# Optimization experiments

Measured on AMD Instinct MI355X. Metric: run time of the kernel, lower is better.

Reference implementation:

```python
import jax, jax.numpy as jnp
import numpy as np

H = 768
NH = 12
HD = H // NH  # 64
WINDOW = 64  # module's self.window_size; band keeps |i-j| <= WINDOW//2


def setup_inputs() -> dict:
    key = jax.random.key(0)
    ks = jax.random.split(key, 9)
    s = 0.02
    return {
        "hidden_states": jax.random.normal(ks[0], (4, 2048, H), dtype=jnp.float32),
        "Wq": jax.random.normal(ks[1], (H, H), dtype=jnp.float32) * s,
        "bq": jnp.zeros((H,), dtype=jnp.float32),
        "Wk": jax.random.normal(ks[2], (H, H), dtype=jnp.float32) * s,
        "bk": jnp.zeros((H,), dtype=jnp.float32),
        "Wv": jax.random.normal(ks[3], (H, H), dtype=jnp.float32) * s,
        "bv": jnp.zeros((H,), dtype=jnp.float32),
        "Wo": jax.random.normal(ks[4], (H, H), dtype=jnp.float32) * s,
        "bo": jnp.zeros((H,), dtype=jnp.float32),
    }


def _attn(hidden_states, Wq, bq, Wk, bk, Wv, bv, Wo, bo):
    B, S, _ = hidden_states.shape
    # projections (torch Linear uses y = x @ W.T + b; here W is stored already transposed)
    q = (hidden_states @ Wq + bq).reshape(B, S, NH, HD).transpose(0, 2, 1, 3)
    k = (hidden_states @ Wk + bk).reshape(B, S, NH, HD).transpose(0, 2, 1, 3)
    v = (hidden_states @ Wv + bv).reshape(B, S, NH, HD).transpose(0, 2, 1, 3)
    # dense scores [B, NH, S, S], faithful to the original O(S^2) computation
    scores = jnp.einsum("bhqd,bhkd->bhqk", q, k) / jnp.sqrt(jnp.float32(HD))
    # sliding-window band mask: keep j in [i - W//2, i + W//2]
    i = jnp.arange(S)[:, None]
    j = jnp.arange(S)[None, :]
    band = jnp.abs(i - j) <= (WINDOW // 2)
    scores = jnp.where(band[None, None, :, :], scores, jnp.float32(-1e9))
    probs = jax.nn.softmax(scores, axis=-1)
    ctx = jnp.einsum("bhqk,bhkd->bhqd", probs, v)
    ctx = ctx.transpose(0, 2, 1, 3).reshape(B, S, H)
    return ctx @ Wo + bo


def reference(hidden_states, Wq, bq, Wk, bk, Wv, bv, Wo, bo):
    return _attn(hidden_states, Wq, bq, Wk, bk, Wv, bv, Wo, bo)
```

## Files before the change

### kernel.cpp

```cpp
#include <hip/hip_runtime.h>
#include <hip/hip_bf16.h>

#define NHEAD 12
#define HD 64
#define SEQ 2048
#define NB 4
#define HDIM 768
#define MTOT (NB * SEQ)

typedef float f32x4 __attribute__((ext_vector_type(4)));
typedef float f32x16 __attribute__((ext_vector_type(16)));
typedef short s16x8 __attribute__((ext_vector_type(8)));
typedef unsigned short u16x8 __attribute__((ext_vector_type(8)));

__device__ inline unsigned short f2bf(float f) {
    union { float f; unsigned u; } v; v.f = f;
    unsigned r = v.u + 0x7fffu + ((v.u >> 16) & 1u);
    return (unsigned short)(r >> 16);
}
__device__ inline float bf2f(unsigned short u) {
    union { unsigned u; float f; } v; v.u = ((unsigned)u) << 16;
    return v.f;
}
__device__ inline unsigned pack_bf2(float a, float b) {
    return (unsigned)f2bf(a) | ((unsigned)f2bf(b) << 16);
}
__device__ inline s16x8 mk_frag(uint2 lo, uint2 hi) {
    union { unsigned u[4]; s16x8 v; } r;
    r.u[0] = lo.x; r.u[1] = lo.y; r.u[2] = hi.x; r.u[3] = hi.y;
    return r.v;
}
__device__ inline void gload_lds16(const unsigned short* g, void* lds_base) {
    __builtin_amdgcn_global_load_lds(
        (const __attribute__((address_space(1))) void*)g,
        (__attribute__((address_space(3))) void*)lds_base, 16, 0, 0);
}

#define MFMA(acc, a, b) \
    acc = __builtin_amdgcn_mfma_f32_16x16x32_bf16((a), (b), (acc), 0, 0, 0)
#define MFMA32(acc, a, b) \
    acc = __builtin_amdgcn_mfma_f32_32x32x16_bf16((a), (b), (acc), 0, 0, 0)

__global__ __launch_bounds__(256) void x_convert(
    const float* __restrict__ X, unsigned short* __restrict__ Xb)
{
    const int i = (blockIdx.x * 256 + threadIdx.x) * 8;
    float4 a = *(const float4*)(X + i);
    float4 b = *(const float4*)(X + i + 4);
    ushort4 wa, wb;
    wa.x = f2bf(a.x); wa.y = f2bf(a.y); wa.z = f2bf(a.z); wa.w = f2bf(a.w);
    wb.x = f2bf(b.x); wb.y = f2bf(b.y); wb.z = f2bf(b.z); wb.w = f2bf(b.w);
    *(ushort4*)(Xb + i) = wa;
    *(ushort4*)(Xb + i + 4) = wb;
}

__global__ __launch_bounds__(256) void w_transpose(
    const float* __restrict__ Wq, const float* __restrict__ Wk,
    const float* __restrict__ Wv, const float* __restrict__ Wo,
    unsigned short* __restrict__ Wt, unsigned short* __restrict__ Wot)
{
    __shared__ __align__(16) unsigned short ts[64][68];
    const int z = blockIdx.z;
    const float* W = (z == 0) ? Wq : (z == 1) ? Wk : (z == 2) ? Wv : Wo;
    unsigned short* D = (z < 3) ? (Wt + (size_t)z * HDIM * HDIM) : Wot;
    const int k0 = blockIdx.x * 64, n0 = blockIdx.y * 64;
    const int t = threadIdx.x;
    const int kr = (t >> 4) * 4;
    const int nc = (t & 15) * 4;
    #pragma unroll
    for (int r = 0; r < 4; r++) {
        float4 v = *(const float4*)(W + (size_t)(k0 + kr + r) * HDIM + n0 + nc);
        ushort4 w;
        w.x = f2bf(v.x); w.y = f2bf(v.y); w.z = f2bf(v.z); w.w = f2bf(v.w);
        *(ushort4*)&ts[kr + r][nc] = w;
    }
    __syncthreads();
    const int nr = t >> 2;
    const int kc = (t & 3) * 16;
    #pragma unroll
    for (int j4 = 0; j4 < 4; j4++) {
        ushort4 w;
        w.x = ts[kc + j4 * 4 + 0][nr];
        w.y = ts[kc + j4 * 4 + 1][nr];
        w.z = ts[kc + j4 * 4 + 2][nr];
        w.w = ts[kc + j4 * 4 + 3][nr];
        *(ushort4*)(D + (size_t)(n0 + nr) * HDIM + k0 + kc + j4 * 4) = w;
    }
}

template<int MODE>
__global__ __launch_bounds__(256) void gemm_kernel(
    const unsigned short* __restrict__ A,
    const unsigned short* __restrict__ Bt,
    const float* __restrict__ bias0, const float* __restrict__ bias1,
    const float* __restrict__ bias2,
    unsigned short* __restrict__ Qb, unsigned short* __restrict__ Kb,
    unsigned short* __restrict__ Vb, float* __restrict__ out)
{
    __shared__ __align__(16) unsigned short As[128 * 64];
    __shared__ __align__(16) unsigned short Bs[128 * 64];

    const int t = threadIdx.x;
    const int lane = t & 63;
    const int wid = t >> 6;
    const int wm = wid >> 1, wn = wid & 1;
    const int l31 = lane & 31;
    const int lh = lane >> 5;

    const int m0 = blockIdx.x * 128;
    const int n0 = blockIdx.y * 128;

    int srow[4], scol[4];
    #pragma unroll
    for (int i = 0; i < 4; i++) {
        const int p = i * 4096 + t * 16;
        const int row = p >> 7;
        const int cb = p & 127;
        srow[i] = row;
        scol[i] = (cb ^ ((row & 7) << 4)) >> 1;
    }

    f32x16 acc[2][2] = {};

    for (int k0 = 0; k0 < HDIM; k0 += 64) {
        __syncthreads();
        #pragma unroll
        for (int i = 0; i < 4; i++)
            gload_lds16(A + (size_t)(m0 + srow[i]) * HDIM + k0 + scol[i],
                        (char*)As + i * 4096 + wid * 1024);
        #pragma unroll
        for (int i = 0; i < 4; i++)
            gload_lds16(Bt + (size_t)(n0 + srow[i]) * HDIM + k0 + scol[i],
                        (char*)Bs + i * 4096 + wid * 1024);
        __syncthreads();

        const int sw = (l31 & 7) << 4;
        #pragma unroll
        for (int kv = 0; kv < 4; kv++) {
            const int cb = (kv * 32 + lh * 16) ^ sw;
            s16x8 a0 = *(const s16x8*)((const char*)As + (wm * 64 +      l31) * 128 + cb);
            s16x8 a1 = *(const s16x8*)((const char*)As + (wm * 64 + 32 + l31) * 128 + cb);
            s16x8 b0 = *(const s16x8*)((const char*)Bs + (wn * 64 +      l31) * 128 + cb);
            s16x8 b1 = *(const s16x8*)((const char*)Bs + (wn * 64 + 32 + l31) * 128 + cb);
            MFMA32(acc[0][0], a0, b0);
            MFMA32(acc[0][1], a0, b1);
            MFMA32(acc[1][0], a1, b0);
            MFMA32(acc[1][1], a1, b1);
        }
    }

    if (MODE == 0) {
        const int z = n0 / HDIM;
        const float* bias = (z == 0) ? bias0 : (z == 1) ? bias1 : bias2;
        const float scale = (z == 0) ? 0.125f : 1.0f;
        unsigned short* dst = (z == 0) ? Qb : (z == 1) ? Kb : Vb;
        #pragma unroll
        for (int fm = 0; fm < 2; fm++) {
            #pragma unroll
            for (int fn = 0; fn < 2; fn++) {
                const int coll = (n0 - z * HDIM) + wn * 64 + fn * 32 + l31;
                const float bc = bias[coll];
                const int h = coll >> 6, d = coll & 63;
                #pragma unroll
                for (int reg = 0; reg < 16; reg++) {
                    const int rowD = (reg & 3) + 8 * (reg >> 2) + 4 * lh;
                    const int m = m0 + wm * 64 + fm * 32 + rowD;
                    const int b = m >> 11, s = m & (SEQ - 1);
                    const size_t idx = (z == 2)
                        ? ((((size_t)b * NHEAD + h) * HD + d) * SEQ + s)
                        : ((((size_t)b * NHEAD + h) * SEQ + s) * HD + d);
                    dst[idx] = f2bf((acc[fm][fn][reg] + bc) * scale);
                }
            }
        }
    } else {
        #pragma unroll
        for (int fm = 0; fm < 2; fm++) {
            #pragma unroll
            for (int fn = 0; fn < 2; fn++) {
                const int col = n0 + wn * 64 + fn * 32 + l31;
                const float bc = bias0[col];
                #pragma unroll
                for (int reg = 0; reg < 16; reg++) {
                    const int rowD = (reg & 3) + 8 * (reg >> 2) + 4 * lh;
                    const int m = m0 + wm * 64 + fm * 32 + rowD;
                    out[(size_t)m * HDIM + col] = acc[fm][fn][reg] + bc;
                }
            }
        }
    }
}

__global__ __launch_bounds__(512) void attn_mfma(
    const unsigned short* __restrict__ Qb, const unsigned short* __restrict__ Kb,
    const unsigned short* __restrict__ Vtg, unsigned short* __restrict__ Cb)
{
    __shared__ __align__(16) unsigned short Ks[192][72];
    __shared__ __align__(16) unsigned short Qs[128][72];
    __shared__ __align__(16) unsigned short Vs[64][208];

    const int t = threadIdx.x;
    const int lane = t & 63;
    const int wq = t >> 6;
    const int woff = wq * 16;
    const int g = lane >> 4, r16 = lane & 15;
    const int q0 = blockIdx.x * 128;
    const int bh = blockIdx.y;
    const int b = bh / NHEAD, h = bh - b * NHEAD;
    const size_t base  = (size_t)bh * SEQ * HD;
    const size_t vbase = (size_t)bh * HD * SEQ;
    const int kstart = q0 - 32;
    const bool interior = (kstart >= 0) && (kstart + 191 < SEQ);

    if (t < 384) {
        const int row = t >> 1, c0 = (t & 1) * 32;
        const int s = kstart + row;
        if (s >= 0 && s < SEQ) {
            const unsigned short* src = Kb + base + (size_t)s * HD + c0;
            #pragma unroll
            for (int j = 0; j < 4; j++)
                *(u16x8*)&Ks[row][c0 + 8 * j] = *(const u16x8*)(src + 8 * j);
        } else {
            const u16x8 z = {};
            #pragma unroll
            for (int j = 0; j < 4; j++)
                *(u16x8*)&Ks[row][c0 + 8 * j] = z;
        }
    }
    {
        const int row = t >> 2, c0 = (t & 3) * 16;
        const unsigned short* src = Qb + base + (size_t)(q0 + row) * HD + c0;
        *(u16x8*)&Qs[row][c0] = *(const u16x8*)src;
        *(u16x8*)&Qs[row][c0 + 8] = *(const u16x8*)(src + 8);
    }
    {
        const int row = t >> 3, c0 = (t & 7) * 24;
        const unsigned short* src = Vtg + vbase + (size_t)row * SEQ + kstart + c0;
        if (interior) {
            #pragma unroll
            for (int j = 0; j < 3; j++)
                *(u16x8*)&Vs[row][c0 + 8 * j] = *(const u16x8*)(src + 8 * j);
        } else {
            for (int e = 0; e < 24; e++) {
                const int s = kstart + c0 + e;
                Vs[row][c0 + e] = (s >= 0 && s < SEQ) ? src[e] : (unsigned short)0;
            }
        }
        if (t < 128) {
            const u16x8 z = {};
            *(u16x8*)&Vs[t >> 1][192 + (t & 1) * 8] = z;
        }
    }
    __syncthreads();

    s16x8 qf[2];
    {
        const unsigned short* p = &Qs[woff + r16][0];
        #pragma unroll
        for (int c = 0; c < 2; c++)
            qf[c] = mk_frag(*(const uint2*)(p + c * 32 + 4 * g),
                            *(const uint2*)(p + c * 32 + 16 + 4 * g));
    }
    f32x4 sacc[5] = {};
    #pragma unroll
    for (int mf = 0; mf < 5; mf++) {
        const unsigned short* p = &Ks[woff + mf * 16 + r16][0];
        #pragma unroll
        for (int c = 0; c < 2; c++) {
            s16x8 kf = mk_frag(*(const uint2*)(p + c * 32 + 4 * g),
                               *(const uint2*)(p + c * 32 + 16 + 4 * g));
            MFMA(sacc[mf], kf, qf[c]);
        }
    }

    float mx = -1e30f;
    #pragma unroll
    for (int mf = 0; mf < 5; mf++) {
        #pragma unroll
        for (int r = 0; r < 4; r++) {
            const int rel = mf * 16 + 4 * g + r - r16;
            const int sg = kstart + woff + mf * 16 + 4 * g + r;
            const bool ok = (rel >= 0) && (rel <= 64) && (sg >= 0) && (sg < SEQ);
            const float v = ok ? sacc[mf][r] : -1e30f;
            sacc[mf][r] = v;
            mx = fmaxf(mx, v);
        }
    }
    mx = fmaxf(mx, __shfl_xor(mx, 16));
    mx = fmaxf(mx, __shfl_xor(mx, 32));
    float l = 0.f;
    #pragma unroll
    for (int mf = 0; mf < 5; mf++) {
        #pragma unroll
        for (int r = 0; r < 4; r++) {
            const float e = __expf(sacc[mf][r] - mx);
            sacc[mf][r] = e;
            l += e;
        }
    }
    l += __shfl_xor(l, 16);
    l += __shfl_xor(l, 32);
    const float inv = 1.f / l;

    s16x8 pf[3];
    #pragma unroll
    for (int c = 0; c < 3; c++) {
        union { unsigned u[4]; s16x8 v; } pv;
        pv.u[0] = pack_bf2(sacc[2 * c][0] * inv, sacc[2 * c][1] * inv);
        pv.u[1] = pack_bf2(sacc[2 * c][2] * inv, sacc[2 * c][3] * inv);
        if (c < 2) {
            pv.u[2] = pack_bf2(sacc[2 * c + 1][0] * inv, sacc[2 * c + 1][1] * inv);
            pv.u[3] = pack_bf2(sacc[2 * c + 1][2] * inv, sacc[2 * c + 1][3] * inv);
        } else {
            pv.u[2] = 0; pv.u[3] = 0;
        }
        pf[c] = pv.v;
    }

    f32x4 cacc[4] = {};
    #pragma unroll
    for (int nf = 0; nf < 4; nf++) {
        const unsigned short* p = &Vs[nf * 16 + r16][woff];
        #pragma unroll
        for (int c = 0; c < 3; c++) {
            s16x8 vf = mk_frag(*(const uint2*)(p + c * 32 + 4 * g),
                               *(const uint2*)(p + c * 32 + 16 + 4 * g));
            MFMA(cacc[nf], pf[c], vf);
        }
    }

    #pragma unroll
    for (int nf = 0; nf < 4; nf++) {
        #pragma unroll
        for (int r = 0; r < 4; r++) {
            const int ql = woff + 4 * g + r;
            const int d = nf * 16 + r16;
            Cb[(((size_t)b * SEQ + q0 + ql) * NHEAD + h) * HD + d] = f2bf(cacc[nf][r]);
        }
    }
}

extern "C" void kernel_launch(void* const* d_in, const int* in_sizes, int n_in,
                              void* d_out, int out_size, void* d_ws, size_t ws_size,
                              hipStream_t stream)
{
    const float* X  = (const float*)d_in[0];
    const float* Wq = (const float*)d_in[1];
    const float* bq = (const float*)d_in[2];
    const float* Wk = (const float*)d_in[3];
    const float* bk = (const float*)d_in[4];
    const float* Wv = (const float*)d_in[5];
    const float* bv = (const float*)d_in[6];
    const float* Wo = (const float*)d_in[7];
    const float* bo = (const float*)d_in[8];
    float* out = (float*)d_out;

    char* ws = (char*)d_ws;
    unsigned short* Xb  = (unsigned short*)ws;
    unsigned short* Cb  = Xb;
    unsigned short* Vt  = (unsigned short*)(ws + 12582912);
    unsigned short* Wtp = (unsigned short*)(ws + 25165824);
    unsigned short* Wot = (unsigned short*)(ws + 28704768);
    unsigned short* Qb  = (unsigned short*)d_out;
    unsigned short* Kb  = (unsigned short*)((char*)d_out + 12582912);

    x_convert<<<dim3(3072), 256, 0, stream>>>(X, Xb);
    w_transpose<<<dim3(12, 12, 4), 256, 0, stream>>>(Wq, Wk, Wv, Wo, Wtp, Wot);
    gemm_kernel<0><<<dim3(64, 18), 256, 0, stream>>>(Xb, Wtp, bq, bk, bv, Qb, Kb, Vt, nullptr);
    attn_mfma<<<dim3(16, 48), 512, 0, stream>>>(Qb, Kb, Vt, Cb);
    gemm_kernel<1><<<dim3(64, 6), 256, 0, stream>>>(Cb, Wot, bo, nullptr, nullptr,
                                                    nullptr, nullptr, nullptr, out);
}
```

Measured before the change: 111.8 us.

## Merge prep kernels, load Q directly into registers, remap attention blocks

Combines the X conversion and weight transpose kernels into one launch, removing one kernel launch. In the attention kernel, Q fragments are read straight from global memory into registers instead of being staged in LDS, which frees LDS and moves the global Q loads ahead of the barrier. K loads are reorganized into coalesced 16-byte chunks across all 512 threads, and block indices are remapped so that consecutive workgroups are spread across heads, presumably for XCD locality. The risk is less coalesced Q fragment loads from global memory.

After: 106.2 us. -5.0%, faster.

```diff
diff --git a/kernel.cpp b/kernel.cpp
--- a/kernel.cpp
+++ b/kernel.cpp
@@ -41,30 +41,36 @@
 #define MFMA32(acc, a, b) \
     acc = __builtin_amdgcn_mfma_f32_32x32x16_bf16((a), (b), (acc), 0, 0, 0)
 
-__global__ __launch_bounds__(256) void x_convert(
-    const float* __restrict__ X, unsigned short* __restrict__ Xb)
-{
-    const int i = (blockIdx.x * 256 + threadIdx.x) * 8;
-    float4 a = *(const float4*)(X + i);
-    float4 b = *(const float4*)(X + i + 4);
-    ushort4 wa, wb;
-    wa.x = f2bf(a.x); wa.y = f2bf(a.y); wa.z = f2bf(a.z); wa.w = f2bf(a.w);
-    wb.x = f2bf(b.x); wb.y = f2bf(b.y); wb.z = f2bf(b.z); wb.w = f2bf(b.w);
-    *(ushort4*)(Xb + i) = wa;
-    *(ushort4*)(Xb + i + 4) = wb;
-}
-
-__global__ __launch_bounds__(256) void w_transpose(
+__global__ __launch_bounds__(256) void prep_kernel(
+    const float* __restrict__ X,
     const float* __restrict__ Wq, const float* __restrict__ Wk,
     const float* __restrict__ Wv, const float* __restrict__ Wo,
+    unsigned short* __restrict__ Xb,
     unsigned short* __restrict__ Wt, unsigned short* __restrict__ Wot)
 {
     __shared__ __align__(16) unsigned short ts[64][68];
-    const int z = blockIdx.z;
+    const int t = threadIdx.x;
+    const int bid = blockIdx.x;
+
+    if (bid < 3072) {
+        const int i = (bid * 256 + t) * 8;
+        float4 a = *(const float4*)(X + i);
+        float4 b = *(const float4*)(X + i + 4);
+        ushort4 wa, wb;
+        wa.x = f2bf(a.x); wa.y = f2bf(a.y); wa.z = f2bf(a.z); wa.w = f2bf(a.w);
+        wb.x = f2bf(b.x); wb.y = f2bf(b.y); wb.z = f2bf(b.z); wb.w = f2bf(b.w);
+        *(ushort4*)(Xb + i) = wa;
+        *(ushort4*)(Xb + i + 4) = wb;
+        return;
+    }
+
+    const int id = bid - 3072;
+    const int z  = id / 144;
+    const int rem = id - z * 144;
+    const int k0 = (rem / 12) * 64, n0 = (rem % 12) * 64;
     const float* W = (z == 0) ? Wq : (z == 1) ? Wk : (z == 2) ? Wv : Wo;
     unsigned short* D = (z < 3) ? (Wt + (size_t)z * HDIM * HDIM) : Wot;
-    const int k0 = blockIdx.x * 64, n0 = blockIdx.y * 64;
-    const int t = threadIdx.x;
+
     const int kr = (t >> 4) * 4;
     const int nc = (t & 15) * 4;
     #pragma unroll
@@ -196,7 +202,6 @@
     const unsigned short* __restrict__ Vtg, unsigned short* __restrict__ Cb)
 {
     __shared__ __align__(16) unsigned short Ks[192][72];
-    __shared__ __align__(16) unsigned short Qs[128][72];
     __shared__ __align__(16) unsigned short Vs[64][208];
 
     const int t = threadIdx.x;
@@ -204,34 +209,30 @@
     const int wq = t >> 6;
     const int woff = wq * 16;
     const int g = lane >> 4, r16 = lane & 15;
-    const int q0 = blockIdx.x * 128;
-    const int bh = blockIdx.y;
+
+    const int lid = blockIdx.y * 16 + blockIdx.x;
+    const int wg = (lid & 7) * 96 + (lid >> 3);
+    const int q0 = (wg & 15) * 128;
+    const int bh = wg >> 4;
+
     const int b = bh / NHEAD, h = bh - b * NHEAD;
     const size_t base  = (size_t)bh * SEQ * HD;
     const size_t vbase = (size_t)bh * HD * SEQ;
     const int kstart = q0 - 32;
     const bool interior = (kstart >= 0) && (kstart + 191 < SEQ);
 
-    if (t < 384) {
-        const int row = t >> 1, c0 = (t & 1) * 32;
+    #pragma unroll
+    for (int i = 0; i < 3; i++) {
+        const int u = i * 512 + t;
+        const int row = u >> 3, c16 = (u & 7) * 8;
         const int s = kstart + row;
         if (s >= 0 && s < SEQ) {
-            const unsigned short* src = Kb + base + (size_t)s * HD + c0;
-            #pragma unroll
-            for (int j = 0; j < 4; j++)
-                *(u16x8*)&Ks[row][c0 + 8 * j] = *(const u16x8*)(src + 8 * j);
+            *(u16x8*)&Ks[row][c16] =
+                *(const u16x8*)(Kb + base + (size_t)s * HD + c16);
         } else {
             const u16x8 z = {};
-            #pragma unroll
-            for (int j = 0; j < 4; j++)
-                *(u16x8*)&Ks[row][c0 + 8 * j] = z;
-        }
-    }
-    {
-        const int row = t >> 2, c0 = (t & 3) * 16;
-        const unsigned short* src = Qb + base + (size_t)(q0 + row) * HD + c0;
-        *(u16x8*)&Qs[row][c0] = *(const u16x8*)src;
-        *(u16x8*)&Qs[row][c0 + 8] = *(const u16x8*)(src + 8);
+            *(u16x8*)&Ks[row][c16] = z;
+        }
     }
     {
         const int row = t >> 3, c0 = (t & 7) * 24;
@@ -251,16 +252,17 @@
             *(u16x8*)&Vs[t >> 1][192 + (t & 1) * 8] = z;
         }
     }
-    __syncthreads();
 
     s16x8 qf[2];
     {
-        const unsigned short* p = &Qs[woff + r16][0];
+        const unsigned short* gq = Qb + base + (size_t)(q0 + woff + r16) * HD;
         #pragma unroll
         for (int c = 0; c < 2; c++)
-            qf[c] = mk_frag(*(const uint2*)(p + c * 32 + 4 * g),
-                            *(const uint2*)(p + c * 32 + 16 + 4 * g));
-    }
+            qf[c] = mk_frag(*(const uint2*)(gq + c * 32 + 4 * g),
+                            *(const uint2*)(gq + c * 32 + 16 + 4 * g));
+    }
+    __syncthreads();
+
     f32x4 sacc[5] = {};
     #pragma unroll
     for (int mf = 0; mf < 5; mf++) {
@@ -364,8 +366,7 @@
     unsigned short* Qb  = (unsigned short*)d_out;
     unsigned short* Kb  = (unsigned short*)((char*)d_out + 12582912);
 
-    x_convert<<<dim3(3072), 256, 0, stream>>>(X, Xb);
-    w_transpose<<<dim3(12, 12, 4), 256, 0, stream>>>(Wq, Wk, Wv, Wo, Wtp, Wot);
+    prep_kernel<<<dim3(3648), 256, 0, stream>>>(X, Wq, Wk, Wv, Wo, Xb, Wtp, Wot);
     gemm_kernel<0><<<dim3(64, 18), 256, 0, stream>>>(Xb, Wtp, bq, bk, bv, Qb, Kb, Vt, nullptr);
     attn_mfma<<<dim3(16, 48), 512, 0, stream>>>(Qb, Kb, Vt, Cb);
     gemm_kernel<1><<<dim3(64, 6), 256, 0, stream>>>(Cb, Wot, bo, nullptr, nullptr,
```
